# Performance work log

Measured on AMD Instinct MI355X. Metric: run time of the kernel, lower is better.

## Reference

```python
import jax, jax.numpy as jnp
import numpy as np

B, Q, DIM, HEADS, HEAD_DIM, KV = 32, 4, 2048, 16, 128, 8192


def setup_inputs() -> dict:
    key = jax.random.key(0)
    ks = jax.random.split(key, 9)
    s = 0.02
    return {
        'x': jax.random.normal(ks[0], (B, Q, DIM), jnp.float32),
        'attn_bias': jax.random.normal(ks[1], (B, HEADS, Q, KV), jnp.float32),
        'cache_k': jax.random.normal(ks[2], (B, KV, HEAD_DIM), jnp.float32),
        'cache_v': jax.random.normal(ks[3], (B, KV, HEAD_DIM), jnp.float32),
        'wq': jax.random.normal(ks[4], (DIM, HEADS, HEAD_DIM), jnp.float32) * s,
        'bq': jnp.zeros((HEADS, HEAD_DIM), jnp.float32),
        'wk': jax.random.normal(ks[5], (DIM, HEAD_DIM), jnp.float32) * s,
        'bk': jnp.zeros((HEAD_DIM,), jnp.float32),
        'wv': jax.random.normal(ks[6], (DIM, HEAD_DIM), jnp.float32) * s,
        'bv': jnp.zeros((HEAD_DIM,), jnp.float32),
        'wo': jax.random.normal(ks[7], (HEADS, HEAD_DIM, DIM), jnp.float32) * s,
        'bo': jnp.zeros((DIM,), jnp.float32),
    }


def reference(x, attn_bias, cache_k, cache_v, wq, bq, wk, bk, wv, bv, wo, bo):
    q_len = x.shape[1]
    # projections (MQA: shared single-head K/V)
    q = jnp.einsum('bqd,dhe->bqhe', x, wq) + bq          # [B,Q,H,hd]
    k_new = x @ wk + bk                                   # [B,Q,hd]
    v_new = x @ wv + bv
    # rolling KV cache update: shift left by q_len, write new tokens at end
    k = jnp.roll(cache_k, -q_len, axis=1).at[:, -q_len:].set(k_new)  # [B,KV,hd]
    v = jnp.roll(cache_v, -q_len, axis=1).at[:, -q_len:].set(v_new)
    scale = 1.0 / (k.shape[-1] ** 0.5)
    p = jnp.einsum('bqhe,bke->bhqk', q, k) * scale        # [B,H,Q,KV]
    a = jax.nn.softmax(p + attn_bias, axis=-1)
    o = jnp.einsum('bhqk,bke->bqhe', a, v)                # [B,Q,H,hd]
    return jnp.einsum('bqhe,hed->bqd', o, wo) + bo        # [B,Q,DIM]
```

## Files before the change

### kernel.cpp

```cpp
#include <hip/hip_runtime.h>
#include <cstddef>
#include <cstdint>

#define BATCH 32
#define QL 4
#define DIM 2048
#define NH 16
#define HD 128
#define KVLEN 8192
#define HQ 64
#define CHUNK 512
#define NCK 16
#define KT 64
#define NT 8

typedef __attribute__((ext_vector_type(8))) short bf16x8;
typedef __attribute__((ext_vector_type(4))) float f32x4;

__device__ __forceinline__ unsigned short cvt_bf16(float f) {
    unsigned int u = __builtin_bit_cast(unsigned int, f);
    u += 0x7fffu + ((u >> 16) & 1u);
    return (unsigned short)(u >> 16);
}
__device__ __forceinline__ unsigned int pack2(float a, float b) {
    return (unsigned int)cvt_bf16(a) | ((unsigned int)cvt_bf16(b) << 16);
}
__device__ __forceinline__ float bf16_to_f32(unsigned short s) {
    unsigned int u = ((unsigned int)s) << 16;
    return __builtin_bit_cast(float, u);
}
__device__ __forceinline__ bf16x8 mk_frag(unsigned int a, unsigned int b,
                                          unsigned int c, unsigned int d) {
    unsigned int t[4] = {a, b, c, d};
    return *(const bf16x8*)t;
}

template<int VARIANT>
__global__ __launch_bounds__(256) void gemm_kernel(
    const float* __restrict__ A,
    const float* __restrict__ w0p, const float* __restrict__ w1p,
    const float* __restrict__ w2p,
    const float* __restrict__ b0p, const float* __restrict__ b1p,
    const float* __restrict__ b2p,
    float* __restrict__ o0, float* __restrict__ o1, float* __restrict__ o2)
{
    const int n0 = blockIdx.x * 64;
    const int m0 = blockIdx.y * 64;
    const int kz = blockIdx.z * 512;
    const int tid = threadIdx.x;
    const int wave = tid >> 6, lane = tid & 63;
    const int l15 = lane & 15, quad = lane >> 4;

    const float* W; const float* Bv; int ldw, nc;
    if (VARIANT == 0) {
        if (n0 >= 2176)      { W = w2p; Bv = b2p; ldw = 128;  nc = n0 - 2176; }
        else if (n0 >= 2048) { W = w1p; Bv = b1p; ldw = 128;  nc = n0 - 2048; }
        else                 { W = w0p; Bv = b0p; ldw = 2048; nc = n0; }
    } else { W = w0p; Bv = b0p; ldw = 2048; nc = n0; }

    __shared__ alignas(16) unsigned short a_s[64][72];
    __shared__ alignas(16) unsigned short w_s[64][68];

    const int wn = tid & 63;
    const int wk0 = (tid >> 6) * 4;

    f32x4 acc[4];
    #pragma unroll
    for (int nt = 0; nt < 4; ++nt) acc[nt] = (f32x4){0.f, 0.f, 0.f, 0.f};

    float4 apre[4];
    float wpre[4][4];

    #pragma unroll
    for (int ii = 0; ii < 4; ++ii) {
        int f = tid + 256 * ii, r = f >> 4, c4 = (f & 15) << 2;
        apre[ii] = *(const float4*)&A[(size_t)(m0 + r) * DIM + kz + c4];
    }
    #pragma unroll
    for (int sub = 0; sub < 4; ++sub) {
        int k0 = kz + wk0 + 16 * sub;
        const float* wp = W + (size_t)k0 * ldw + nc + wn;
        #pragma unroll
        for (int j = 0; j < 4; ++j) wpre[sub][j] = wp[(size_t)j * ldw];
    }

    for (int it = 0; it < 8; ++it) {
        __syncthreads();
        #pragma unroll
        for (int ii = 0; ii < 4; ++ii) {
            int f = tid + 256 * ii, r = f >> 4, c4 = (f & 15) << 2;
            *(uint2*)&a_s[r][c4] =
                make_uint2(pack2(apre[ii].x, apre[ii].y), pack2(apre[ii].z, apre[ii].w));
        }
        #pragma unroll
        for (int sub = 0; sub < 4; ++sub) {
            int k0 = wk0 + 16 * sub;
            *(uint2*)&w_s[wn][k0] =
                make_uint2(pack2(wpre[sub][0], wpre[sub][1]),
                           pack2(wpre[sub][2], wpre[sub][3]));
        }
        __syncthreads();
        if (it + 1 < 8) {
            const int kb = kz + (it + 1) * 64;
            #pragma unroll
            for (int ii = 0; ii < 4; ++ii) {
                int f = tid + 256 * ii, r = f >> 4, c4 = (f & 15) << 2;
                apre[ii] = *(const float4*)&A[(size_t)(m0 + r) * DIM + kb + c4];
            }
            #pragma unroll
            for (int sub = 0; sub < 4; ++sub) {
                int k0 = kb + wk0 + 16 * sub;
                const float* wp = W + (size_t)k0 * ldw + nc + wn;
                #pragma unroll
                for (int j = 0; j < 4; ++j) wpre[sub][j] = wp[(size_t)j * ldw];
            }
        }
        #pragma unroll
        for (int kf = 0; kf < 2; ++kf) {
            bf16x8 af = *(const bf16x8*)&a_s[16 * wave + l15][kf * 32 + quad * 8];
            #pragma unroll
            for (int nt = 0; nt < 4; ++nt) {
                uint2 lo = *(const uint2*)&w_s[nt * 16 + l15][kf * 32 + quad * 8];
                uint2 hi = *(const uint2*)&w_s[nt * 16 + l15][kf * 32 + quad * 8 + 4];
                bf16x8 wf = mk_frag(lo.x, lo.y, hi.x, hi.y);
                acc[nt] = __builtin_amdgcn_mfma_f32_16x16x32_bf16(af, wf, acc[nt], 0, 0, 0);
            }
        }
    }
    const bool addb = (blockIdx.z == 0);
    #pragma unroll
    for (int nt = 0; nt < 4; ++nt)
        #pragma unroll
        for (int reg = 0; reg < 4; ++reg) {
            int row = m0 + 16 * wave + quad * 4 + reg;
            int col = n0 + nt * 16 + l15;
            float s = acc[nt][reg];
            if (VARIANT == 1) {
                atomicAdd(&o0[(size_t)row * DIM + col], s + (addb ? Bv[col] : 0.f));
            } else {
                int b = row >> 2, q = row & 3;
                if (col < 2048) {
                    int h = col >> 7, e = col & 127;
                    atomicAdd(&o0[((size_t)(b * 64 + h * 4 + q)) * 128 + e],
                              s + (addb ? b0p[col] : 0.f));
                } else if (col < 2176) {
                    int e = col - 2048;
                    atomicAdd(&o1[(size_t)row * 128 + e], s + (addb ? b1p[e] : 0.f));
                } else {
                    int e = col - 2176;
                    atomicAdd(&o2[(size_t)row * 128 + e], s + (addb ? b2p[e] : 0.f));
                }
            }
        }
}


#define PREFETCH_KV(tb_)                                                      \
    do {                                                                      \
        _Pragma("unroll")                                                     \
        for (int i = 0; i < 8; ++i) {                                         \
            int f = tid + 256 * i;                                            \
            int row = f >> 5, e0 = (f & 31) << 2;                             \
            int kv = (tb_) + row;                                             \
            const float* pk = (kv < KVLEN - QL)                               \
                ? cachek + ((size_t)b * KVLEN + kv + QL) * HD + e0            \
                : kws + ((size_t)b * QL + (kv - (KVLEN - QL))) * HD + e0;     \
            kpre[i] = *(const float4*)pk;                                     \
        }                                                                     \
        _Pragma("unroll")                                                     \
        for (int i = 0; i < 8; ++i) {                                         \
            int kv0 = (tb_) + (vkq + 2 * i) * 4;                              \
            _Pragma("unroll")                                                 \
            for (int j = 0; j < 4; ++j) {                                     \
                int kv = kv0 + j;                                             \
                const float* pv = (kv < KVLEN - QL)                           \
                    ? cachev + ((size_t)b * KVLEN + kv + QL) * HD + ve        \
                    : vws + ((size_t)b * QL + (kv - (KVLEN - QL))) * HD + ve; \
                vpre[i][j] = *pv;                                             \
            }                                                                 \
        }                                                                     \
    } while (0)

#define PREFETCH_B(toff_)                                                     \
    do {                                                                      \
        _Pragma("unroll")                                                     \
        for (int nt = 0; nt < 4; ++nt)                                        \
            _Pragma("unroll")                                                 \
            for (int reg = 0; reg < 4; ++reg)                                 \
                bpre[nt * 4 + reg] = bptr[reg][(toff_) + nt * 16];            \
    } while (0)

#define STORE_LDS(ks_, vs_)                                                   \
    do {                                                                      \
        _Pragma("unroll")                                                     \
        for (int i = 0; i < 8; ++i) {                                         \
            int f = tid + 256 * i;                                            \
            int row = f >> 5, e0 = (f & 31) << 2;                             \
            *(uint2*)&ks_[row][e0] =                                          \
                make_uint2(pack2(kpre[i].x, kpre[i].y),                       \
                           pack2(kpre[i].z, kpre[i].w));                      \
        }                                                                     \
        _Pragma("unroll")                                                     \
        for (int i = 0; i < 8; ++i) {                                         \
            int kv0 = (vkq + 2 * i) * 4;                                      \
            *(uint2*)&vs_[ve][kv0] =                                          \
                make_uint2(pack2(vpre[i][0], vpre[i][1]),                     \
                           pack2(vpre[i][2], vpre[i][3]));                    \
        }                                                                     \
    } while (0)

#define COMPUTE_TILE(bias_, ks_, vs_)                                         \
    do {                                                                      \
        f32x4 sacc[4];                                                        \
        _Pragma("unroll")                                                     \
        for (int nt = 0; nt < 4; ++nt) sacc[nt] = (f32x4){0.f, 0.f, 0.f, 0.f};\
        __builtin_amdgcn_s_setprio(1);                                        \
        _Pragma("unroll")                                                     \
        for (int kf = 0; kf < 4; ++kf) {                                      \
            _Pragma("unroll")                                                 \
            for (int nt = 0; nt < 4; ++nt) {                                  \
                bf16x8 kfb = *(const bf16x8*)&ks_[nt * 16 + l15][kf * 32 + quad * 8]; \
                sacc[nt] = __builtin_amdgcn_mfma_f32_16x16x32_bf16(qf[kf], kfb, sacc[nt], 0, 0, 0); \
            }                                                                 \
        }                                                                     \
        __builtin_amdgcn_s_setprio(0);                                        \
        _Pragma("unroll")                                                     \
        for (int nt = 0; nt < 4; ++nt)                                        \
            _Pragma("unroll")                                                 \
            for (int reg = 0; reg < 4; ++reg) {                               \
                float s = sacc[nt][reg] * scale + bias_[nt * 4 + reg];        \
                float p = __expf(s);                                          \
                unsigned short pb = cvt_bf16(p);                              \
                lrow[reg] += bf16_to_f32(pb);                                 \
                p_s[wave][quad * 4 + reg][nt * 16 + l15] = pb;                \
            }                                                                 \
        __builtin_amdgcn_s_setprio(1);                                        \
        _Pragma("unroll")                                                     \
        for (int kfp = 0; kfp < 2; ++kfp) {                                   \
            uint2 plo = *(const uint2*)&p_s[wave][l15][kfp * 32 + quad * 8];  \
            uint2 phi = *(const uint2*)&p_s[wave][l15][kfp * 32 + quad * 8 + 4]; \
            bf16x8 pf = mk_frag(plo.x, plo.y, phi.x, phi.y);                  \
            _Pragma("unroll")                                                 \
            for (int n8 = 0; n8 < 8; ++n8) {                                  \
                uint2 vlo = *(const uint2*)&vs_[n8 * 16 + l15][kfp * 32 + quad * 8]; \
                uint2 vhi = *(const uint2*)&vs_[n8 * 16 + l15][kfp * 32 + quad * 8 + 4]; \
                bf16x8 vf = mk_frag(vlo.x, vlo.y, vhi.x, vhi.y);              \
                oa[n8] = __builtin_amdgcn_mfma_f32_16x16x32_bf16(pf, vf, oa[n8], 0, 0, 0); \
            }                                                                 \
        }                                                                     \
        __builtin_amdgcn_s_setprio(0);                                        \
    } while (0)

__global__ __launch_bounds__(256, 2) void attn_kernel(
    const float* __restrict__ qws, const float* __restrict__ kws,
    const float* __restrict__ vws,
    const float* __restrict__ cachek, const float* __restrict__ cachev,
    const float* __restrict__ abias,
    float* __restrict__ opart, float* __restrict__ lpart)
{
    const int ck = blockIdx.x;
    const int b  = blockIdx.y;
    const int tid = threadIdx.x;
    const int wave = tid >> 6, lane = tid & 63;
    const int l15 = lane & 15, quad = lane >> 4;
    const float scale = 0.08838834764831845f;

    __shared__ alignas(16) unsigned short k_s0[KT][136];
    __shared__ alignas(16) unsigned short k_s1[KT][136];
    __shared__ alignas(16) unsigned short v_s0[HD][68];
    __shared__ alignas(16) unsigned short v_s1[HD][68];
    __shared__ alignas(16) unsigned short p_s[4][16][72];

    bf16x8 qf[4];
    {
        const float* qrow = qws + ((size_t)b * HQ + 16 * wave + l15) * HD;
        #pragma unroll
        for (int kf = 0; kf < 4; ++kf) {
            float4 f0 = *(const float4*)&qrow[kf * 32 + quad * 8];
            float4 f1 = *(const float4*)&qrow[kf * 32 + quad * 8 + 4];
            qf[kf] = mk_frag(pack2(f0.x, f0.y), pack2(f0.z, f0.w),
                             pack2(f1.x, f1.y), pack2(f1.z, f1.w));
        }
    }

    const int kbase0 = ck * CHUNK;
    const int ve = tid & 127;
    const int vkq = (tid >> 7);

    const float* bptr[4];
    #pragma unroll
    for (int reg = 0; reg < 4; ++reg) {
        int hq = 16 * wave + quad * 4 + reg;
        int h = hq >> 2, q = hq & 3;
        bptr[reg] = abias + (((size_t)(b * NH + h)) * QL + q) * KVLEN + kbase0 + l15;
    }

    float4 kpre[8];
    float vpre[8][4];
    float bpre[16];

    PREFETCH_KV(kbase0);
    STORE_LDS(k_s0, v_s0);
    PREFETCH_KV(kbase0 + KT);
    PREFETCH_B(0);

    f32x4 oa[8];
    #pragma unroll
    for (int n8 = 0; n8 < 8; ++n8) oa[n8] = (f32x4){0.f, 0.f, 0.f, 0.f};
    float lrow[4] = {0.f, 0.f, 0.f, 0.f};

    for (int tt = 0; tt < NT; tt += 2) {
        {
            __syncthreads();
            float bias[16];
            #pragma unroll
            for (int j = 0; j < 16; ++j) bias[j] = bpre[j];
            PREFETCH_B((tt + 1) * KT);
            COMPUTE_TILE(bias, k_s0, v_s0);
            STORE_LDS(k_s1, v_s1);
            if (tt + 2 < NT) PREFETCH_KV(kbase0 + (tt + 2) * KT);
        }
        {
            __syncthreads();
            float bias[16];
            #pragma unroll
            for (int j = 0; j < 16; ++j) bias[j] = bpre[j];
            if (tt + 2 < NT) PREFETCH_B((tt + 2) * KT);
            COMPUTE_TILE(bias, k_s1, v_s1);
            if (tt + 2 < NT) {
                STORE_LDS(k_s0, v_s0);
                if (tt + 3 < NT) PREFETCH_KV(kbase0 + (tt + 3) * KT);
            }
        }
    }
    #pragma unroll
    for (int reg = 0; reg < 4; ++reg) {
        float v = lrow[reg];
        v += __shfl_xor(v, 1);
        v += __shfl_xor(v, 2);
        v += __shfl_xor(v, 4);
        v += __shfl_xor(v, 8);
        lrow[reg] = v;
    }
    const size_t obase = ((size_t)(b * NCK + ck)) * HQ * HD;
    #pragma unroll
    for (int n8 = 0; n8 < 8; ++n8)
        #pragma unroll
        for (int reg = 0; reg < 4; ++reg) {
            int hq = 16 * wave + quad * 4 + reg;
            int e = n8 * 16 + l15;
            opart[obase + (size_t)hq * HD + e] = oa[n8][reg];
        }
    if (l15 == 0) {
        #pragma unroll
        for (int reg = 0; reg < 4; ++reg) {
            int hq = 16 * wave + quad * 4 + reg;
            lpart[(size_t)(b * NCK + ck) * HQ + hq] = lrow[reg];
        }
    }
}

__global__ __launch_bounds__(128) void combine_kernel(
    const float* __restrict__ opart, const float* __restrict__ lpart,
    float* __restrict__ ored, float* __restrict__ outz)
{
    const int bh = blockIdx.x;
    const int b = bh >> 6, hq = bh & 63;
    const int e = threadIdx.x;
    outz[(size_t)bh * 128 + e] = 0.f;
    float lt = 0.f, ov = 0.f;
    #pragma unroll
    for (int c = 0; c < NCK; ++c) {
        lt += lpart[(b * NCK + c) * HQ + hq];
        ov += opart[((size_t)(b * NCK + c) * HQ + hq) * HD + e];
    }
    int h = hq >> 2, q = hq & 3;
    ored[(size_t)(b * QL + q) * DIM + h * HD + e] = ov / lt;
}

extern "C" void kernel_launch(void* const* d_in, const int* in_sizes, int n_in,
                              void* d_out, int out_size, void* d_ws, size_t ws_size,
                              hipStream_t stream)
{
    const float* x   = (const float*)d_in[0];
    const float* ab  = (const float*)d_in[1];
    const float* cK  = (const float*)d_in[2];
    const float* cV  = (const float*)d_in[3];
    const float* wq  = (const float*)d_in[4];
    const float* bq  = (const float*)d_in[5];
    const float* wk  = (const float*)d_in[6];
    const float* bk  = (const float*)d_in[7];
    const float* wv  = (const float*)d_in[8];
    const float* bv  = (const float*)d_in[9];
    const float* wo  = (const float*)d_in[10];
    const float* bo  = (const float*)d_in[11];
    float* out = (float*)d_out;

    float* ws   = (float*)d_ws;
    float* wsq  = ws;
    float* wsk  = wsq + 262144;
    float* wsv  = wsk + 16384;
    float* wsop = wsv + 16384;
    float* wsl  = wsop + 4194304;
    float* wsor = wsl + 32768;

    hipMemsetAsync(ws, 0, (size_t)(262144 + 16384 + 16384) * sizeof(float),
                   stream);

    gemm_kernel<0><<<dim3(36, 2, 4), 256, 0, stream>>>(
        x, wq, wk, wv, bq, bk, bv, wsq, wsk, wsv);
    attn_kernel<<<dim3(NCK, BATCH), 256, 0, stream>>>(
        wsq, wsk, wsv, cK, cV, ab, wsop, wsl);
    combine_kernel<<<BATCH * HQ, 128, 0, stream>>>(wsop, wsl, wsor, out);
    gemm_kernel<1><<<dim3(32, 2, 4), 256, 0, stream>>>(
        wsor, wo, nullptr, nullptr, bo, nullptr, nullptr, out, nullptr, nullptr);
}
```

Baseline: 398.6 us.

## Fuse split-KV combine into attention atomics and output GEMM prologue

Removes the combine kernel. The attention chunks now atomically accumulate unnormalized outputs and row sums into a single zeroed buffer, and the output projection GEMM reads that buffer with the head/query remap and applies the 1/l normalization while loading A. Zeroing of the final output moves into the first GEMM, and the K and V prefetch/store macros are split and interleaved to spread global loads. This saves a launch and the partial-buffer round trip, at the cost of float atomic contention (16 chunks per element) and non-deterministic summation order.

```diff
diff --git a/kernel.cpp b/kernel.cpp
--- a/kernel.cpp
+++ b/kernel.cpp
@@ -42,7 +42,8 @@
     const float* __restrict__ w2p,
     const float* __restrict__ b0p, const float* __restrict__ b1p,
     const float* __restrict__ b2p,
-    float* __restrict__ o0, float* __restrict__ o1, float* __restrict__ o2)
+    float* __restrict__ o0, float* __restrict__ o1, float* __restrict__ o2,
+    float* __restrict__ zout)
 {
     const int n0 = blockIdx.x * 64;
     const int m0 = blockIdx.y * 64;
@@ -51,12 +52,23 @@
     const int wave = tid >> 6, lane = tid & 63;
     const int l15 = lane & 15, quad = lane >> 4;
 
+    if (VARIANT == 0) {
+        int gbid = (blockIdx.z * 2 + blockIdx.y) * 36 + blockIdx.x;
+        int base = gbid * 256 + tid;
+        #pragma unroll
+        for (int i = 0; i < 4; ++i) {
+            int idx = base + 73728 * i;
+            if (idx < 262144) zout[idx] = 0.f;
+        }
+    }
+
     const float* W; const float* Bv; int ldw, nc;
     if (VARIANT == 0) {
         if (n0 >= 2176)      { W = w2p; Bv = b2p; ldw = 128;  nc = n0 - 2176; }
         else if (n0 >= 2048) { W = w1p; Bv = b1p; ldw = 128;  nc = n0 - 2048; }
         else                 { W = w0p; Bv = b0p; ldw = 2048; nc = n0; }
     } else { W = w0p; Bv = b0p; ldw = 2048; nc = n0; }
+    const float* Lp = w1p;
 
     __shared__ alignas(16) unsigned short a_s[64][72];
     __shared__ alignas(16) unsigned short w_s[64][68];
@@ -74,7 +86,16 @@
     #pragma unroll
     for (int ii = 0; ii < 4; ++ii) {
         int f = tid + 256 * ii, r = f >> 4, c4 = (f & 15) << 2;
-        apre[ii] = *(const float4*)&A[(size_t)(m0 + r) * DIM + kz + c4];
+        int row = m0 + r, cc = kz + c4;
+        if (VARIANT == 1) {
+            int bb = row >> 2, q = row & 3, h = cc >> 7, e0 = cc & 127;
+            int hq = h * 4 + q;
+            float4 v = *(const float4*)&A[((size_t)(bb * 64 + hq)) * 128 + e0];
+            float linv = 1.0f / Lp[bb * 64 + hq];
+            apre[ii] = make_float4(v.x * linv, v.y * linv, v.z * linv, v.w * linv);
+        } else {
+            apre[ii] = *(const float4*)&A[(size_t)row * DIM + cc];
+        }
     }
     #pragma unroll
     for (int sub = 0; sub < 4; ++sub) {
@@ -105,7 +126,16 @@
             #pragma unroll
             for (int ii = 0; ii < 4; ++ii) {
                 int f = tid + 256 * ii, r = f >> 4, c4 = (f & 15) << 2;
-                apre[ii] = *(const float4*)&A[(size_t)(m0 + r) * DIM + kb + c4];
+                int row = m0 + r, cc = kb + c4;
+                if (VARIANT == 1) {
+                    int bb = row >> 2, q = row & 3, h = cc >> 7, e0 = cc & 127;
+                    int hq = h * 4 + q;
+                    float4 v = *(const float4*)&A[((size_t)(bb * 64 + hq)) * 128 + e0];
+                    float linv = 1.0f / Lp[bb * 64 + hq];
+                    apre[ii] = make_float4(v.x * linv, v.y * linv, v.z * linv, v.w * linv);
+                } else {
+                    apre[ii] = *(const float4*)&A[(size_t)row * DIM + cc];
+                }
             }
             #pragma unroll
             for (int sub = 0; sub < 4; ++sub) {
@@ -155,7 +185,7 @@
 }
 
 
-#define PREFETCH_KV(tb_)                                                      \
+#define PREFETCH_K(tb_)                                                       \
     do {                                                                      \
         _Pragma("unroll")                                                     \
         for (int i = 0; i < 8; ++i) {                                         \
@@ -167,6 +197,10 @@
                 : kws + ((size_t)b * QL + (kv - (KVLEN - QL))) * HD + e0;     \
             kpre[i] = *(const float4*)pk;                                     \
         }                                                                     \
+    } while (0)
+
+#define PREFETCH_V(tb_)                                                       \
+    do {                                                                      \
         _Pragma("unroll")                                                     \
         for (int i = 0; i < 8; ++i) {                                         \
             int kv0 = (tb_) + (vkq + 2 * i) * 4;                              \
@@ -190,7 +224,7 @@
                 bpre[nt * 4 + reg] = bptr[reg][(toff_) + nt * 16];            \
     } while (0)
 
-#define STORE_LDS(ks_, vs_)                                                   \
+#define STORE_K(ks_)                                                          \
     do {                                                                      \
         _Pragma("unroll")                                                     \
         for (int i = 0; i < 8; ++i) {                                         \
@@ -200,6 +234,10 @@
                 make_uint2(pack2(kpre[i].x, kpre[i].y),                       \
                            pack2(kpre[i].z, kpre[i].w));                      \
         }                                                                     \
+    } while (0)
+
+#define STORE_V(vs_)                                                          \
+    do {                                                                      \
         _Pragma("unroll")                                                     \
         for (int i = 0; i < 8; ++i) {                                         \
             int kv0 = (vkq + 2 * i) * 4;                                      \
@@ -256,7 +294,7 @@
     const float* __restrict__ vws,
     const float* __restrict__ cachek, const float* __restrict__ cachev,
     const float* __restrict__ abias,
-    float* __restrict__ opart, float* __restrict__ lpart)
+    float* __restrict__ oacc, float* __restrict__ lacc)
 {
     const int ck = blockIdx.x;
     const int b  = blockIdx.y;
@@ -299,9 +337,12 @@
     float vpre[8][4];
     float bpre[16];
 
-    PREFETCH_KV(kbase0);
-    STORE_LDS(k_s0, v_s0);
-    PREFETCH_KV(kbase0 + KT);
+    PREFETCH_K(kbase0);
+    PREFETCH_V(kbase0);
+    STORE_K(k_s0);
+    STORE_V(v_s0);
+    PREFETCH_K(kbase0 + KT);
+    PREFETCH_V(kbase0 + KT);
     PREFETCH_B(0);
 
     f32x4 oa[8];
@@ -317,8 +358,10 @@
             for (int j = 0; j < 16; ++j) bias[j] = bpre[j];
             PREFETCH_B((tt + 1) * KT);
             COMPUTE_TILE(bias, k_s0, v_s0);
-            STORE_LDS(k_s1, v_s1);
-            if (tt + 2 < NT) PREFETCH_KV(kbase0 + (tt + 2) * KT);
+            STORE_K(k_s1);
+            if (tt + 2 < NT) PREFETCH_K(kbase0 + (tt + 2) * KT);
+            STORE_V(v_s1);
+            if (tt + 2 < NT) PREFETCH_V(kbase0 + (tt + 2) * KT);
         }
         {
             __syncthreads();
@@ -328,8 +371,10 @@
             if (tt + 2 < NT) PREFETCH_B((tt + 2) * KT);
             COMPUTE_TILE(bias, k_s1, v_s1);
             if (tt + 2 < NT) {
-                STORE_LDS(k_s0, v_s0);
-                if (tt + 3 < NT) PREFETCH_KV(kbase0 + (tt + 3) * KT);
+                STORE_K(k_s0);
+                if (tt + 3 < NT) PREFETCH_K(kbase0 + (tt + 3) * KT);
+                STORE_V(v_s0);
+                if (tt + 3 < NT) PREFETCH_V(kbase0 + (tt + 3) * KT);
             }
         }
     }
@@ -342,40 +387,22 @@
         v += __shfl_xor(v, 8);
         lrow[reg] = v;
     }
-    const size_t obase = ((size_t)(b * NCK + ck)) * HQ * HD;
+    const size_t abase = (size_t)b * HQ * HD;
     #pragma unroll
     for (int n8 = 0; n8 < 8; ++n8)
         #pragma unroll
         for (int reg = 0; reg < 4; ++reg) {
             int hq = 16 * wave + quad * 4 + reg;
             int e = n8 * 16 + l15;
-            opart[obase + (size_t)hq * HD + e] = oa[n8][reg];
+            atomicAdd(&oacc[abase + (size_t)hq * HD + e], oa[n8][reg]);
         }
     if (l15 == 0) {
         #pragma unroll
         for (int reg = 0; reg < 4; ++reg) {
             int hq = 16 * wave + quad * 4 + reg;
-            lpart[(size_t)(b * NCK + ck) * HQ + hq] = lrow[reg];
-        }
-    }
-}
-
-__global__ __launch_bounds__(128) void combine_kernel(
-    const float* __restrict__ opart, const float* __restrict__ lpart,
-    float* __restrict__ ored, float* __restrict__ outz)
-{
-    const int bh = blockIdx.x;
-    const int b = bh >> 6, hq = bh & 63;
-    const int e = threadIdx.x;
-    outz[(size_t)bh * 128 + e] = 0.f;
-    float lt = 0.f, ov = 0.f;
-    #pragma unroll
-    for (int c = 0; c < NCK; ++c) {
-        lt += lpart[(b * NCK + c) * HQ + hq];
-        ov += opart[((size_t)(b * NCK + c) * HQ + hq) * HD + e];
-    }
-    int h = hq >> 2, q = hq & 3;
-    ored[(size_t)(b * QL + q) * DIM + h * HD + e] = ov / lt;
+            atomicAdd(&lacc[b * HQ + hq], lrow[reg]);
+        }
+    }
 }
 
 extern "C" void kernel_launch(void* const* d_in, const int* in_sizes, int n_in,
@@ -400,18 +427,18 @@
     float* wsq  = ws;
     float* wsk  = wsq + 262144;
     float* wsv  = wsk + 16384;
-    float* wsop = wsv + 16384;
-    float* wsl  = wsop + 4194304;
-    float* wsor = wsl + 32768;
-
-    hipMemsetAsync(ws, 0, (size_t)(262144 + 16384 + 16384) * sizeof(float),
-                   stream);
+    float* oacc = wsv + 16384;
+    float* lacc = oacc + 262144;
+
+    hipMemsetAsync(ws, 0,
+        (size_t)(262144 + 16384 + 16384 + 262144 + 2048) * sizeof(float),
+        stream);
 
     gemm_kernel<0><<<dim3(36, 2, 4), 256, 0, stream>>>(
-        x, wq, wk, wv, bq, bk, bv, wsq, wsk, wsv);
+        x, wq, wk, wv, bq, bk, bv, wsq, wsk, wsv, out);
     attn_kernel<<<dim3(NCK, BATCH), 256, 0, stream>>>(
-        wsq, wsk, wsv, cK, cV, ab, wsop, wsl);
-    combine_kernel<<<BATCH * HQ, 128, 0, stream>>>(wsop, wsl, wsor, out);
+        wsq, wsk, wsv, cK, cV, ab, oacc, lacc);
     gemm_kernel<1><<<dim3(32, 2, 4), 256, 0, stream>>>(
-        wsor, wo, nullptr, nullptr, bo, nullptr, nullptr, out, nullptr, nullptr);
-}
+        oacc, wo, lacc, nullptr, bo, nullptr, nullptr, out, nullptr, nullptr,
+        nullptr);
+}
```

After: 396.0 us. Within noise of the previous version (-0.7%).

## Fuse split-KV combine into attention kernel via last-block atomic counter

Applied to the files above, without the earlier changes.

Removes the separate combine kernel launch. Each attention block increments a per-batch counter, and the last block to finish a batch sums the partial outputs and row sums across the 16 chunks with float4 loads, then writes the normalized result. Zeroing of the output buffer, which the split-K output GEMM accumulates into, moves into the first GEMM kernel. This saves one launch and its scheduling gap but serializes the reduction onto one block per batch, a tail the last blocks must finish.

```diff
diff --git a/kernel.cpp b/kernel.cpp
--- a/kernel.cpp
+++ b/kernel.cpp
@@ -42,7 +42,8 @@
     const float* __restrict__ w2p,
     const float* __restrict__ b0p, const float* __restrict__ b1p,
     const float* __restrict__ b2p,
-    float* __restrict__ o0, float* __restrict__ o1, float* __restrict__ o2)
+    float* __restrict__ o0, float* __restrict__ o1, float* __restrict__ o2,
+    float* __restrict__ zout)
 {
     const int n0 = blockIdx.x * 64;
     const int m0 = blockIdx.y * 64;
@@ -50,6 +51,16 @@
     const int tid = threadIdx.x;
     const int wave = tid >> 6, lane = tid & 63;
     const int l15 = lane & 15, quad = lane >> 4;
+
+    if (VARIANT == 0) {
+        int gbid = (blockIdx.z * 2 + blockIdx.y) * 36 + blockIdx.x;
+        int base = gbid * 256 + tid;
+        #pragma unroll
+        for (int i = 0; i < 4; ++i) {
+            int idx = base + 73728 * i;
+            if (idx < 262144) zout[idx] = 0.f;
+        }
+    }
 
     const float* W; const float* Bv; int ldw, nc;
     if (VARIANT == 0) {
@@ -256,7 +267,8 @@
     const float* __restrict__ vws,
     const float* __restrict__ cachek, const float* __restrict__ cachev,
     const float* __restrict__ abias,
-    float* __restrict__ opart, float* __restrict__ lpart)
+    float* __restrict__ opart, float* __restrict__ lpart,
+    float* __restrict__ wsor, int* __restrict__ cnt)
 {
     const int ck = blockIdx.x;
     const int b  = blockIdx.y;
@@ -270,6 +282,8 @@
     __shared__ alignas(16) unsigned short v_s0[HD][68];
     __shared__ alignas(16) unsigned short v_s1[HD][68];
     __shared__ alignas(16) unsigned short p_s[4][16][72];
+    __shared__ float ls_s[HQ];
+    __shared__ int lastFlag;
 
     bf16x8 qf[4];
     {
@@ -358,24 +372,37 @@
             lpart[(size_t)(b * NCK + ck) * HQ + hq] = lrow[reg];
         }
     }
-}
-
-__global__ __launch_bounds__(128) void combine_kernel(
-    const float* __restrict__ opart, const float* __restrict__ lpart,
-    float* __restrict__ ored, float* __restrict__ outz)
-{
-    const int bh = blockIdx.x;
-    const int b = bh >> 6, hq = bh & 63;
-    const int e = threadIdx.x;
-    outz[(size_t)bh * 128 + e] = 0.f;
-    float lt = 0.f, ov = 0.f;
-    #pragma unroll
-    for (int c = 0; c < NCK; ++c) {
-        lt += lpart[(b * NCK + c) * HQ + hq];
-        ov += opart[((size_t)(b * NCK + c) * HQ + hq) * HD + e];
-    }
-    int h = hq >> 2, q = hq & 3;
-    ored[(size_t)(b * QL + q) * DIM + h * HD + e] = ov / lt;
+    __threadfence();
+    if (tid == 0)
+        lastFlag = (atomicAdd(&cnt[b], 1) == NCK - 1);
+    __syncthreads();
+    if (lastFlag) {
+        __threadfence();
+        if (tid < HQ) {
+            float s = 0.f;
+            #pragma unroll
+            for (int c = 0; c < NCK; ++c)
+                s += lpart[(size_t)(b * NCK + c) * HQ + tid];
+            ls_s[tid] = s;
+        }
+        __syncthreads();
+        #pragma unroll
+        for (int i = 0; i < 8; ++i) {
+            int f4 = tid + 256 * i;
+            int hq = f4 >> 5, e4 = (f4 & 31) << 2;
+            float sx = 0.f, sy = 0.f, sz = 0.f, sw = 0.f;
+            #pragma unroll
+            for (int c = 0; c < NCK; ++c) {
+                float4 v = *(const float4*)&opart[
+                    (((size_t)(b * NCK + c)) * HQ + hq) * HD + e4];
+                sx += v.x; sy += v.y; sz += v.z; sw += v.w;
+            }
+            float inv = 1.0f / ls_s[hq];
+            int h = hq >> 2, q = hq & 3;
+            *(float4*)&wsor[((size_t)(b * QL + q)) * DIM + h * HD + e4] =
+                make_float4(sx * inv, sy * inv, sz * inv, sw * inv);
+        }
+    }
 }
 
 extern "C" void kernel_launch(void* const* d_in, const int* in_sizes, int n_in,
@@ -396,22 +423,23 @@
     const float* bo  = (const float*)d_in[11];
     float* out = (float*)d_out;
 
-    float* ws   = (float*)d_ws;
-    float* wsq  = ws;
-    float* wsk  = wsq + 262144;
-    float* wsv  = wsk + 16384;
-    float* wsop = wsv + 16384;
-    float* wsl  = wsop + 4194304;
-    float* wsor = wsl + 32768;
-
-    hipMemsetAsync(ws, 0, (size_t)(262144 + 16384 + 16384) * sizeof(float),
+    float* ws    = (float*)d_ws;
+    float* wsq   = ws;
+    float* wsk   = wsq + 262144;
+    float* wsv   = wsk + 16384;
+    int*   cnt   = (int*)(wsv + 16384);
+    float* opart = wsv + 16384 + 64;
+    float* lpart = opart + 4194304;
+    float* wsor  = lpart + 32768;
+
+    hipMemsetAsync(ws, 0, (size_t)(262144 + 16384 + 16384 + 64) * sizeof(float),
                    stream);
 
     gemm_kernel<0><<<dim3(36, 2, 4), 256, 0, stream>>>(
-        x, wq, wk, wv, bq, bk, bv, wsq, wsk, wsv);
+        x, wq, wk, wv, bq, bk, bv, wsq, wsk, wsv, out);
     attn_kernel<<<dim3(NCK, BATCH), 256, 0, stream>>>(
-        wsq, wsk, wsv, cK, cV, ab, wsop, wsl);
-    combine_kernel<<<BATCH * HQ, 128, 0, stream>>>(wsop, wsl, wsor, out);
+        wsq, wsk, wsv, cK, cV, ab, opart, lpart, wsor, cnt);
     gemm_kernel<1><<<dim3(32, 2, 4), 256, 0, stream>>>(
-        wsor, wo, nullptr, nullptr, bo, nullptr, nullptr, out, nullptr, nullptr);
-}
+        wsor, wo, nullptr, nullptr, bo, nullptr, nullptr, out, nullptr, nullptr,
+        nullptr);
+}
```

After: 498.8 us. 25.1% more time.
